# Kernel tuning notes

Hardware: AMD Instinct MI355X
Metric: run time of the kernel (lower is better)

The kernel has to match this reference:

```python
import math
import jax, jax.numpy as jnp
import numpy as np
from math import factorial as fact

RS_IN = [(8, 0), (8, 1)]
RS_OUT = [(8, 0), (8, 1)]
N_PATH = 384
HIDDEN = 64
B, N_OUT_PTS, N_IN_PTS = 2, 256, 256

def _lfilters(l_in, l_out, lmax=10):
    return [l for l in range(abs(l_in - l_out), l_in + l_out + 1) if l <= lmax]

# ---- Clebsch-Gordan / Wigner-3j in the real spherical-harmonic basis ----
def _cg(j1, m1, j2, m2, j3, m3):
    if m1 + m2 != m3:
        return 0.0
    kmin = max(0, j2 - j3 - m1, j1 - j3 + m2)
    kmax = min(j1 + j2 - j3, j1 - m1, j2 + m2)
    if kmax < kmin:
        return 0.0
    pre = math.sqrt((2 * j3 + 1) * fact(j3 + j1 - j2) * fact(j3 - j1 + j2) * fact(j1 + j2 - j3) / fact(j1 + j2 + j3 + 1))
    pre *= math.sqrt(fact(j3 + m3) * fact(j3 - m3) * fact(j1 - m1) * fact(j1 + m1) * fact(j2 - m2) * fact(j2 + m2))
    s = sum((-1) ** k / (fact(k) * fact(j1 + j2 - j3 - k) * fact(j1 - m1 - k) * fact(j2 + m2 - k) * fact(j3 - j2 + m1 + k) * fact(j3 - j1 - m2 + k)) for k in range(kmin, kmax + 1))
    return pre * s

def _wigner3j(j1, j2, j3):
    W = np.zeros((2 * j1 + 1, 2 * j2 + 1, 2 * j3 + 1))
    for m1 in range(-j1, j1 + 1):
        for m2 in range(-j2, j2 + 1):
            m3 = -(m1 + m2)
            if abs(m3) <= j3:
                W[m1 + j1, m2 + j2, m3 + j3] = (-1) ** (j1 - j2 - m3) / math.sqrt(2 * j3 + 1) * _cg(j1, m1, j2, m2, j3, -m3)
    return W

def _A(l):
    # change of basis real<->complex SH: Y^real_a = sum_m A[a, m] Y^complex_m
    A = np.zeros((2 * l + 1, 2 * l + 1), dtype=np.complex128)
    A[l, l] = 1.0
    for m in range(1, l + 1):
        A[l + m, l + m] = (-1) ** m / math.sqrt(2)
        A[l + m, l - m] = 1.0 / math.sqrt(2)
        A[l - m, l - m] = 1j / math.sqrt(2)
        A[l - m, l + m] = -1j * (-1) ** m / math.sqrt(2)
    return A

def _real_cg(l1, l2, l3):
    W = _wigner3j(l1, l2, l3).astype(np.complex128)
    Q = np.einsum('am,bn,cp,mnp->abc', _A(l1).conj(), _A(l2).conj(), _A(l3).conj(), W)
    v = Q.flat[int(np.argmax(np.abs(Q)))]
    if abs(v) > 1e-12:
        Q = Q * (v.conjugate() / abs(v))  # rotate global phase so tensor is real
    assert np.abs(Q.imag).max() < 1e-8
    return Q.real.astype(np.float32)

# ---- real spherical harmonics of unit directions, l = 0, 1, 2 ----
_C0 = 0.28209479177387814
_C1 = 0.4886025119029199
_C2A = 1.0925484305920792
_C2B = 0.31539156525252005
_C2C = 0.5462742152960396

def _sh(xyz):
    r = jnp.linalg.norm(xyz, axis=-1, keepdims=True)
    u = xyz / jnp.maximum(r, 1e-12)
    x, y, z = u[..., 0], u[..., 1], u[..., 2]
    Y0 = _C0 * jnp.ones_like(x)[..., None]
    Y1 = _C1 * jnp.stack([y, z, x], axis=-1)
    Y2 = jnp.stack([_C2A * x * y, _C2A * y * z, _C2B * (3.0 * z * z - 1.0), _C2A * x * z, _C2C * (x * x - y * y)], axis=-1)
    return {0: Y0, 1: Y1, 2: Y2}


def setup_inputs() -> dict:
    key = jax.random.key(0)
    ks = jax.random.split(key, 3)
    dm = jax.random.normal(ks[0], (B, N_OUT_PTS, N_IN_PTS, 3), dtype=jnp.float32)
    W1 = 0.1 * jax.random.normal(ks[1], (1, HIDDEN), dtype=jnp.float32)
    b1 = jnp.zeros((HIDDEN,), dtype=jnp.float32)
    W2 = (1.0 / math.sqrt(HIDDEN)) * jax.random.normal(ks[2], (HIDDEN, N_PATH), dtype=jnp.float32)
    b2 = jnp.zeros((N_PATH,), dtype=jnp.float32)
    Q00 = jnp.asarray(_real_cg(0, 0, 0))  # (1,1,1)
    Q01 = jnp.asarray(_real_cg(0, 1, 1))  # (1,3,3)
    Q10 = jnp.asarray(_real_cg(1, 0, 1))  # (3,1,3)
    Q11 = jnp.asarray(np.concatenate([_real_cg(1, 1, l) for l in (0, 1, 2)], axis=2))  # (3,3,9)
    return {"difference_matrix": dm, "W1": W1, "b1": b1, "W2": W2, "b2": b2, "Q00": Q00, "Q01": Q01, "Q10": Q10, "Q11": Q11}


def reference(difference_matrix, W1, b1, W2, b2, Q00, Q01, Q10, Q11):
    Bb, No, Ni, _ = difference_matrix.shape
    Ys = _sh(difference_matrix)                       # l -> [B, No, Ni, 2l+1]
    radii = jnp.linalg.norm(difference_matrix, axis=-1)
    h = jax.nn.relu(radii[..., None] * W1[0] + b1)    # radial MLP
    weights = h @ W2 + b2                             # [B, No, Ni, N_PATH]
    Qs = {(0, 0): Q00, (0, 1): Q01, (1, 0): Q10, (1, 1): Q11}
    begin_w = 0
    rows = []
    for i, (mul_out, l_out) in enumerate(RS_OUT):
        num = sum(mul_in * len(_lfilters(l_in, l_out)) for mul_in, l_in in RS_IN) * Ni
        cols = []
        for j, (mul_in, l_in) in enumerate(RS_IN):
            lfs = _lfilters(l_in, l_out)
            n = mul_out * mul_in * len(lfs)
            w = weights[..., begin_w:begin_w + n].reshape(Bb, No, Ni, mul_out, mul_in, len(lfs))
            begin_w += n
            Q = Qs[(i, j)]
            K = 0.0
            off = 0
            for k, lf in enumerate(lfs):
                Qk = Q[:, :, off:off + 2 * lf + 1]
                off += 2 * lf + 1
                # i=m_out, j=m_in, r=m_filter, b n m = batch/N_out/N_in, u v = mul_out/mul_in
                K = K + jnp.einsum('ijr,bnmr,bnmuv->uivjbnm', Qk, Ys[lf], w[..., k])
            K = K * (math.sqrt(2 * l_in + 1) * math.sqrt(4.0 * math.pi) / math.sqrt(num))
            cols.append(K.reshape(mul_out * (2 * l_out + 1), mul_in * (2 * l_in + 1), Bb, No, Ni))
        rows.append(jnp.concatenate(cols, axis=1))
    return jnp.concatenate(rows, axis=0)  # [n_out, n_in, B, N_out, N_in]
```

## Files before the change

### kernel.cpp

```cpp
#include <hip/hip_runtime.h>
#include <math.h>

namespace {

typedef float f32x4 __attribute__((ext_vector_type(4)));

constexpr int kPts   = 2 * 256 * 256;
constexpr int kPlane = kPts;
constexpr int kHid   = 64;
constexpr int kPath  = 384;
constexpr int kG     = 8;
constexpr int kUvPer = 64 / kG;

constexpr size_t kWsV    = (size_t)kPath * kHid;
constexpr size_t kWsFlag = kWsV + kPath;
constexpr size_t kWsNeedBytes = (kWsFlag + 1) * sizeof(float);

__global__ void prep_kernel(const float* __restrict__ W1,
                            const float* __restrict__ b1,
                            const float* __restrict__ W2,
                            float* __restrict__ W2T,
                            float* __restrict__ V,
                            unsigned* __restrict__ flag)
{
    int t = blockIdx.x * blockDim.x + threadIdx.x;
    if (t < kPath * kHid) {
        int p = t >> 6, i = t & 63;
        W2T[t] = W2[i * kPath + p];
    }
    if (t < kPath) {
        float acc = 0.f;
        for (int i = 0; i < kHid; ++i)
            acc += fmaxf(W1[i], 0.f) * W2[i * kPath + t];
        V[t] = acc;
    }
    if (t == 0) {
        unsigned f = 1u;
        for (int i = 0; i < kHid; ++i)
            if (b1[i] != 0.f) f = 0u;
        *flag = f;
    }
}

template <bool USE_WS>
__global__ __launch_bounds__(256)
void se3_kernel(const float* __restrict__ dm,
                const float* __restrict__ W1,
                const float* __restrict__ b1,
                const float* __restrict__ W2,
                const float* __restrict__ b2,
                const float* __restrict__ Q00,
                const float* __restrict__ Q01,
                const float* __restrict__ Q10,
                const float* __restrict__ Q11,
                const float* __restrict__ W2T,
                const float* __restrict__ V,
                const unsigned* __restrict__ flag,
                float* __restrict__ out)
{
    const int g   = blockIdx.x * blockDim.x + threadIdx.x;
    const int uv0 = blockIdx.y * kUvPer;

    const f32x4* dmv = reinterpret_cast<const f32x4*>(dm) + 3 * (size_t)g;
    f32x4 f0 = dmv[0], f1 = dmv[1], f2 = dmv[2];
    float px[4] = { f0.x, f0.w, f1.z, f2.y };
    float py[4] = { f0.y, f1.x, f1.w, f2.z };
    float pz[4] = { f0.z, f1.y, f2.x, f2.w };

    float r[4], ux[4], uy[4], uz[4];
#pragma unroll
    for (int p = 0; p < 4; ++p) {
        r[p] = sqrtf(px[p] * px[p] + py[p] * py[p] + pz[p] * pz[p]);
        float inv = 1.0f / fmaxf(r[p], 1e-12f);
        ux[p] = px[p] * inv; uy[p] = py[p] * inv; uz[p] = pz[p] * inv;
    }

    const float Y0 = 0.28209479177387814f;
    const float c1 = 0.4886025119029199f;
    float Y10[4], Y11[4], Y12[4], Y2[5][4];
#pragma unroll
    for (int p = 0; p < 4; ++p) {
        Y10[p] = c1 * uy[p];
        Y11[p] = c1 * uz[p];
        Y12[p] = c1 * ux[p];
        Y2[0][p] = 1.0925484305920792f * ux[p] * uy[p];
        Y2[1][p] = 1.0925484305920792f * uy[p] * uz[p];
        Y2[2][p] = 0.31539156525252005f * (3.f * uz[p] * uz[p] - 1.f);
        Y2[3][p] = 1.0925484305920792f * ux[p] * uz[p];
        Y2[4][p] = 0.5462742152960396f * (ux[p] * ux[p] - uy[p] * uy[p]);
    }

    constexpr float kS4pi = 3.5449077018110318f;
    constexpr float kSq3  = 1.7320508075688772f;
    const float n00 = kS4pi / 64.f;
    const float n01 = kSq3 * kS4pi / 64.f;
    const float n10 = kS4pi / 90.50966799187809f;
    const float n11 = kSq3 * kS4pi / 90.50966799187809f;

    const float s00 = n00 * Q00[0] * Y0;
    float G0[9];
#pragma unroll
    for (int e = 0; e < 9; ++e) G0[e] = n11 * Q11[e * 9 + 0] * Y0;

    float g01[3][4], g10[3][4], G1[9][4], G2[9][4];
#pragma unroll
    for (int jc = 0; jc < 3; ++jc) {
        float q0 = Q01[jc * 3 + 0], q1 = Q01[jc * 3 + 1], q2 = Q01[jc * 3 + 2];
#pragma unroll
        for (int p = 0; p < 4; ++p)
            g01[jc][p] = n01 * (q0 * Y10[p] + q1 * Y11[p] + q2 * Y12[p]);
    }
#pragma unroll
    for (int ir = 0; ir < 3; ++ir) {
        float q0 = Q10[ir * 3 + 0], q1 = Q10[ir * 3 + 1], q2 = Q10[ir * 3 + 2];
#pragma unroll
        for (int p = 0; p < 4; ++p)
            g10[ir][p] = n10 * (q0 * Y10[p] + q1 * Y11[p] + q2 * Y12[p]);
    }
#pragma unroll
    for (int e = 0; e < 9; ++e) {
        const float* q = Q11 + e * 9;
        float q1 = q[1], q2 = q[2], q3 = q[3];
        float q4 = q[4], q5 = q[5], q6 = q[6], q7 = q[7], q8 = q[8];
#pragma unroll
        for (int p = 0; p < 4; ++p) {
            G1[e][p] = n11 * (q1 * Y10[p] + q2 * Y11[p] + q3 * Y12[p]);
            G2[e][p] = n11 * (q4 * Y2[0][p] + q5 * Y2[1][p] + q6 * Y2[2][p] +
                              q7 * Y2[3][p] + q8 * Y2[4][p]);
        }
    }

    float* __restrict__ obase = out + 4 * (size_t)g;
    auto stf = [&](int row, const float* v4) {
        f32x4 q;
        q.x = v4[0]; q.y = v4[1]; q.z = v4[2]; q.w = v4[3];
        *reinterpret_cast<f32x4*>(obase + (size_t)row * kPlane) = q;
    };

    auto emit = [&](int uv, const float* w00, const float* w01,
                    const float* w10, const float* w110,
                    const float* w111, const float* w112) {
        const int u = uv >> 3, v = uv & 7;
        const int rowu = u * 32;
        float tmp[4];
#pragma unroll
        for (int p = 0; p < 4; ++p) tmp[p] = s00 * w00[p];
        stf(rowu + v, tmp);
#pragma unroll
        for (int jc = 0; jc < 3; ++jc) {
#pragma unroll
            for (int p = 0; p < 4; ++p) tmp[p] = g01[jc][p] * w01[p];
            stf(rowu + 8 + v * 3 + jc, tmp);
        }
#pragma unroll
        for (int ir = 0; ir < 3; ++ir) {
            const int rowb = (8 + u * 3 + ir) * 32;
#pragma unroll
            for (int p = 0; p < 4; ++p) tmp[p] = g10[ir][p] * w10[p];
            stf(rowb + v, tmp);
#pragma unroll
            for (int jc = 0; jc < 3; ++jc) {
                const int e = ir * 3 + jc;
#pragma unroll
                for (int p = 0; p < 4; ++p)
                    tmp[p] = fmaf(G0[e], w110[p],
                              fmaf(G1[e][p], w111[p], G2[e][p] * w112[p]));
                stf(rowb + 8 + v * 3 + jc, tmp);
            }
        }
    };

    bool fast = false;
    if constexpr (USE_WS) fast = (*flag != 0u);

    if (USE_WS && fast) {
#pragma unroll 1
        for (int t = 0; t < kUvPer; ++t) {
            const int uv = uv0 + t;
            float v00 = V[uv],            c00 = b2[uv];
            float v01 = V[64 + uv],       c01 = b2[64 + uv];
            float v10 = V[128 + uv],      c10 = b2[128 + uv];
            float v50 = V[192 + 3 * uv],  c50 = b2[192 + 3 * uv];
            float v51 = V[193 + 3 * uv],  c51 = b2[193 + 3 * uv];
            float v52 = V[194 + 3 * uv],  c52 = b2[194 + 3 * uv];
            float w00[4], w01[4], w10[4], w110[4], w111[4], w112[4];
#pragma unroll
            for (int p = 0; p < 4; ++p) {
                w00[p]  = fmaf(r[p], v00, c00);
                w01[p]  = fmaf(r[p], v01, c01);
                w10[p]  = fmaf(r[p], v10, c10);
                w110[p] = fmaf(r[p], v50, c50);
                w111[p] = fmaf(r[p], v51, c51);
                w112[p] = fmaf(r[p], v52, c52);
            }
            emit(uv, w00, w01, w10, w110, w111, w112);
        }
    } else {
#pragma unroll 1
        for (int t = 0; t < kUvPer; ++t) {
            const int uv = uv0 + t;
            float a00[4], a01[4], a10[4], a110[4], a111[4], a112[4];
#pragma unroll
            for (int p = 0; p < 4; ++p) {
                a00[p]  = b2[uv];
                a01[p]  = b2[64 + uv];
                a10[p]  = b2[128 + uv];
                a110[p] = b2[192 + 3 * uv];
                a111[p] = b2[193 + 3 * uv];
                a112[p] = b2[194 + 3 * uv];
            }
#pragma unroll 1
            for (int i = 0; i < kHid; ++i) {
                float w1i = W1[i], b1i = b1[i];
                float c00, c01, c10, c50, c51, c52;
                if constexpr (USE_WS) {
                    c00 = W2T[(size_t)uv * 64 + i];
                    c01 = W2T[(size_t)(64 + uv) * 64 + i];
                    c10 = W2T[(size_t)(128 + uv) * 64 + i];
                    c50 = W2T[(size_t)(192 + 3 * uv) * 64 + i];
                    c51 = W2T[(size_t)(193 + 3 * uv) * 64 + i];
                    c52 = W2T[(size_t)(194 + 3 * uv) * 64 + i];
                } else {
                    const float* row = W2 + (size_t)i * kPath;
                    c00 = row[uv];
                    c01 = row[64 + uv];
                    c10 = row[128 + uv];
                    c50 = row[192 + 3 * uv];
                    c51 = row[193 + 3 * uv];
                    c52 = row[194 + 3 * uv];
                }
#pragma unroll
                for (int p = 0; p < 4; ++p) {
                    float hi = fmaxf(fmaf(r[p], w1i, b1i), 0.f);
                    a00[p]  = fmaf(hi, c00, a00[p]);
                    a01[p]  = fmaf(hi, c01, a01[p]);
                    a10[p]  = fmaf(hi, c10, a10[p]);
                    a110[p] = fmaf(hi, c50, a110[p]);
                    a111[p] = fmaf(hi, c51, a111[p]);
                    a112[p] = fmaf(hi, c52, a112[p]);
                }
            }
            emit(uv, a00, a01, a10, a110, a111, a112);
        }
    }
}

}

extern "C" void kernel_launch(void* const* d_in, const int* in_sizes, int n_in,
                              void* d_out, int out_size, void* d_ws, size_t ws_size,
                              hipStream_t stream)
{
    const float* dm  = (const float*)d_in[0];
    const float* W1  = (const float*)d_in[1];
    const float* b1  = (const float*)d_in[2];
    const float* W2  = (const float*)d_in[3];
    const float* b2  = (const float*)d_in[4];
    const float* Q00 = (const float*)d_in[5];
    const float* Q01 = (const float*)d_in[6];
    const float* Q10 = (const float*)d_in[7];
    const float* Q11 = (const float*)d_in[8];
    float* out = (float*)d_out;

    const int threads = 256;
    dim3 grid(kPts / 4 / threads, kG);

    if (ws_size >= kWsNeedBytes) {
        float* W2T = (float*)d_ws;
        float* V   = W2T + kWsV;
        unsigned* flag = (unsigned*)(W2T + kWsFlag);
        prep_kernel<<<(kPath * kHid + threads - 1) / threads, threads, 0, stream>>>(
            W1, b1, W2, W2T, V, flag);
        se3_kernel<true><<<grid, threads, 0, stream>>>(
            dm, W1, b1, W2, b2, Q00, Q01, Q10, Q11, W2T, V, flag, out);
    } else {
        se3_kernel<false><<<grid, threads, 0, stream>>>(
            dm, W1, b1, W2, b2, Q00, Q01, Q10, Q11, nullptr, nullptr, nullptr, out);
    }
}
```

Baseline: 117.3 us.

## Split SE3 kernel into staged geometry, weight precompute and per-path sweep kernels

Adds a stage kernel that writes each point's radius and unit direction to the workspace once, along with the folded MLP vector and the zero-bias flag. A sweep kernel then gives each block one (u,v) path pair and a 4096-point segment, and writes 16 output rows with coalesced scalar stores. The aim is to spread output writes across a wider grid and cut redundant spherical-harmonic recomputation. When bias is nonzero, a separate kernel stages the full MLP outputs into a large workspace buffer of about 200 MB. If the workspace is smaller than that, execution falls back to a mono kernel that always evaluates the full MLP and no longer has the zero-bias shortcut.

Result: faster. 113.9 us (-2.9%).

```diff
diff --git a/kernel.cpp b/kernel.cpp
--- a/kernel.cpp
+++ b/kernel.cpp
@@ -4,62 +4,234 @@
 namespace {
 
 typedef float f32x4 __attribute__((ext_vector_type(4)));
-
-constexpr int kPts   = 2 * 256 * 256;
-constexpr int kPlane = kPts;
-constexpr int kHid   = 64;
-constexpr int kPath  = 384;
-constexpr int kG     = 8;
-constexpr int kUvPer = 64 / kG;
-
-constexpr size_t kWsV    = (size_t)kPath * kHid;
-constexpr size_t kWsFlag = kWsV + kPath;
-constexpr size_t kWsNeedBytes = (kWsFlag + 1) * sizeof(float);
-
-__global__ void prep_kernel(const float* __restrict__ W1,
-                            const float* __restrict__ b1,
-                            const float* __restrict__ W2,
-                            float* __restrict__ W2T,
-                            float* __restrict__ V,
-                            unsigned* __restrict__ flag)
-{
-    int t = blockIdx.x * blockDim.x + threadIdx.x;
-    if (t < kPath * kHid) {
-        int p = t >> 6, i = t & 63;
-        W2T[t] = W2[i * kPath + p];
-    }
-    if (t < kPath) {
-        float acc = 0.f;
-        for (int i = 0; i < kHid; ++i)
-            acc += fmaxf(W1[i], 0.f) * W2[i * kPath + t];
-        V[t] = acc;
-    }
-    if (t == 0) {
-        unsigned f = 1u;
-        for (int i = 0; i < kHid; ++i)
-            if (b1[i] != 0.f) f = 0u;
-        *flag = f;
-    }
-}
-
-template <bool USE_WS>
+typedef float f32x2 __attribute__((ext_vector_type(2)));
+
+constexpr int kPts  = 2 * 256 * 256;
+constexpr int kHid  = 64;
+constexpr int kPath = 384;
+
+constexpr size_t kVOff    = (size_t)kPts * 4;
+constexpr size_t kFlagOff = kVOff + kPath;
+constexpr size_t kWOff    = kVOff + 512;
+constexpr size_t kWFloats = 64ull * kPts * 6;
+constexpr size_t kNeedBytes = (kWOff + kWFloats) * 4;
+
+constexpr float kY0   = 0.28209479177387814f;
+constexpr float kC1   = 0.4886025119029199f;
+constexpr float kC2A  = 1.0925484305920792f;
+constexpr float kC2B  = 0.31539156525252005f;
+constexpr float kC2C  = 0.5462742152960396f;
+constexpr float kS4pi = 3.5449077018110318f;
+constexpr float kSq3  = 1.7320508075688772f;
+constexpr float kN00  = kS4pi / 64.f;
+constexpr float kN01  = kSq3 * kS4pi / 64.f;
+constexpr float kN10  = kS4pi / 90.50966799187809f;
+constexpr float kN11  = kSq3 * kS4pi / 90.50966799187809f;
+
 __global__ __launch_bounds__(256)
-void se3_kernel(const float* __restrict__ dm,
-                const float* __restrict__ W1,
-                const float* __restrict__ b1,
-                const float* __restrict__ W2,
-                const float* __restrict__ b2,
-                const float* __restrict__ Q00,
-                const float* __restrict__ Q01,
-                const float* __restrict__ Q10,
-                const float* __restrict__ Q11,
-                const float* __restrict__ W2T,
-                const float* __restrict__ V,
-                const unsigned* __restrict__ flag,
-                float* __restrict__ out)
+void stage_kernel(const float* __restrict__ dm,
+                  const float* __restrict__ W1,
+                  const float* __restrict__ b1,
+                  const float* __restrict__ W2,
+                  f32x4* __restrict__ ru,
+                  float* __restrict__ V,
+                  unsigned* __restrict__ flag)
+{
+    const int pt = blockIdx.x * 256 + threadIdx.x;
+    float dx = dm[3 * pt + 0], dy = dm[3 * pt + 1], dz = dm[3 * pt + 2];
+    float r  = sqrtf(dx * dx + dy * dy + dz * dz);
+    float inv = 1.0f / fmaxf(r, 1e-12f);
+    f32x4 q; q.x = r; q.y = dx * inv; q.z = dy * inv; q.w = dz * inv;
+    ru[pt] = q;
+
+    if (blockIdx.x == 0) {
+        for (int p = threadIdx.x; p < kPath; p += 256) {
+            float acc = 0.f;
+            for (int i = 0; i < kHid; ++i)
+                acc += fmaxf(W1[i], 0.f) * W2[i * kPath + p];
+            V[p] = acc;
+        }
+        if (threadIdx.x == 0) {
+            unsigned f = 1u;
+            for (int i = 0; i < kHid; ++i)
+                if (b1[i] != 0.f) f = 0u;
+            *flag = f;
+        }
+    }
+}
+
+__global__ __launch_bounds__(256)
+void wstage_kernel(const float* __restrict__ W1,
+                   const float* __restrict__ b1,
+                   const float* __restrict__ W2,
+                   const float* __restrict__ b2,
+                   const f32x4* __restrict__ ru,
+                   const unsigned* __restrict__ flag,
+                   float* __restrict__ wout)
+{
+    if (*flag) return;
+    const int pt = blockIdx.x * 256 + threadIdx.x;
+    const float r = ru[pt].x;
+    float h[kHid];
+#pragma unroll
+    for (int i = 0; i < kHid; ++i)
+        h[i] = fmaxf(fmaf(r, W1[i], b1[i]), 0.f);
+
+#pragma unroll 1
+    for (int uv = 0; uv < 64; ++uv) {
+        const int p[6] = { uv, 64 + uv, 128 + uv,
+                           192 + 3 * uv, 193 + 3 * uv, 194 + 3 * uv };
+        float acc[6];
+#pragma unroll
+        for (int c = 0; c < 6; ++c) acc[c] = b2[p[c]];
+#pragma unroll 1
+        for (int i = 0; i < kHid; ++i) {
+            const float* row = W2 + (size_t)i * kPath;
+#pragma unroll
+            for (int c = 0; c < 6; ++c) acc[c] = fmaf(h[i], row[p[c]], acc[c]);
+        }
+        float* o = wout + ((size_t)uv * kPts + pt) * 6;
+#pragma unroll
+        for (int c = 0; c < 6; ++c) o[c] = acc[c];
+    }
+}
+
+__global__ __launch_bounds__(256)
+void sweep_kernel(const float* __restrict__ Q00,
+                  const float* __restrict__ Q01,
+                  const float* __restrict__ Q10,
+                  const float* __restrict__ Q11,
+                  const float* __restrict__ b2,
+                  const f32x4* __restrict__ ru,
+                  const float* __restrict__ V,
+                  const unsigned* __restrict__ flag,
+                  const float* __restrict__ wstaged,
+                  float* __restrict__ out)
+{
+    const int seg = blockIdx.x;
+    const int uv  = blockIdx.y;
+    const int u = uv >> 3, v = uv & 7;
+
+    const float s00p = kN00 * Q00[0] * kY0;
+    float a01[3][3], a10[3][3], g0c[9], a11[9][3], b11[9][5];
+    const float c2s[5] = { kC2A, kC2A, kC2B, kC2A, kC2C };
+#pragma unroll
+    for (int jc = 0; jc < 3; ++jc)
+#pragma unroll
+        for (int m = 0; m < 3; ++m)
+            a01[jc][m] = kN01 * kC1 * Q01[jc * 3 + m];
+#pragma unroll
+    for (int ir = 0; ir < 3; ++ir)
+#pragma unroll
+        for (int m = 0; m < 3; ++m)
+            a10[ir][m] = kN10 * kC1 * Q10[ir * 3 + m];
+#pragma unroll
+    for (int e = 0; e < 9; ++e) {
+        g0c[e] = kN11 * kY0 * Q11[e * 9 + 0];
+#pragma unroll
+        for (int m = 0; m < 3; ++m) a11[e][m] = kN11 * kC1 * Q11[e * 9 + 1 + m];
+#pragma unroll
+        for (int m = 0; m < 5; ++m) b11[e][m] = kN11 * c2s[m] * Q11[e * 9 + 4 + m];
+    }
+
+    const bool fast = (*flag != 0u);
+    const int pw[6] = { uv, 64 + uv, 128 + uv,
+                        192 + 3 * uv, 193 + 3 * uv, 194 + 3 * uv };
+    float vv[6], cc[6];
+#pragma unroll
+    for (int c = 0; c < 6; ++c) { vv[c] = V[pw[c]]; cc[c] = b2[pw[c]]; }
+
+    int pr[16];
+    pr[0] = u * 32 + v;
+#pragma unroll
+    for (int jc = 0; jc < 3; ++jc) pr[1 + jc] = u * 32 + 8 + v * 3 + jc;
+#pragma unroll
+    for (int ir = 0; ir < 3; ++ir) pr[4 + ir] = (8 + u * 3 + ir) * 32 + v;
+#pragma unroll
+    for (int e = 0; e < 9; ++e)
+        pr[7 + e] = (8 + u * 3 + (e / 3)) * 32 + 8 + v * 3 + (e % 3);
+
+    const size_t segbase = (size_t)seg * 4096 + threadIdx.x;
+
+#pragma unroll 1
+    for (int batch = 0; batch < 4; ++batch) {
+        const size_t p0 = segbase + (size_t)batch * 1024;
+
+        float bs[4][8], w_[4][6];
+#pragma unroll
+        for (int k = 0; k < 4; ++k) {
+            f32x4 q = ru[p0 + k * 256];
+            float r = q.x, x = q.y, y = q.z, z = q.w;
+            bs[k][0] = y;  bs[k][1] = z;  bs[k][2] = x;
+            bs[k][3] = x * y;
+            bs[k][4] = y * z;
+            bs[k][5] = fmaf(3.f * z, z, -1.f);
+            bs[k][6] = x * z;
+            bs[k][7] = fmaf(x, x, -(y * y));
+            if (fast) {
+#pragma unroll
+                for (int c = 0; c < 6; ++c) w_[k][c] = fmaf(r, vv[c], cc[c]);
+            } else {
+                const float* wp = wstaged + ((size_t)uv * kPts + (p0 + k * 256)) * 6;
+#pragma unroll
+                for (int c = 0; c < 6; ++c) w_[k][c] = wp[c];
+            }
+        }
+
+#pragma unroll
+        for (int k = 0; k < 4; ++k)
+            out[(size_t)pr[0] * kPts + p0 + k * 256] = s00p * w_[k][0];
+
+#pragma unroll
+        for (int jc = 0; jc < 3; ++jc) {
+#pragma unroll
+            for (int k = 0; k < 4; ++k) {
+                float g = fmaf(a01[jc][2], bs[k][2],
+                           fmaf(a01[jc][1], bs[k][1], a01[jc][0] * bs[k][0]));
+                out[(size_t)pr[1 + jc] * kPts + p0 + k * 256] = g * w_[k][1];
+            }
+        }
+#pragma unroll
+        for (int ir = 0; ir < 3; ++ir) {
+#pragma unroll
+            for (int k = 0; k < 4; ++k) {
+                float g = fmaf(a10[ir][2], bs[k][2],
+                           fmaf(a10[ir][1], bs[k][1], a10[ir][0] * bs[k][0]));
+                out[(size_t)pr[4 + ir] * kPts + p0 + k * 256] = g * w_[k][2];
+            }
+        }
+#pragma unroll
+        for (int e = 0; e < 9; ++e) {
+#pragma unroll
+            for (int k = 0; k < 4; ++k) {
+                float lin = fmaf(a11[e][2], bs[k][2],
+                             fmaf(a11[e][1], bs[k][1], a11[e][0] * bs[k][0]));
+                float quad = b11[e][0] * bs[k][3];
+#pragma unroll
+                for (int m = 1; m < 5; ++m)
+                    quad = fmaf(b11[e][m], bs[k][3 + m], quad);
+                float val = fmaf(g0c[e], w_[k][3],
+                             fmaf(lin, w_[k][4], quad * w_[k][5]));
+                out[(size_t)pr[7 + e] * kPts + p0 + k * 256] = val;
+            }
+        }
+    }
+}
+
+__global__ __launch_bounds__(256)
+void mono_kernel(const float* __restrict__ dm,
+                 const float* __restrict__ W1,
+                 const float* __restrict__ b1,
+                 const float* __restrict__ W2,
+                 const float* __restrict__ b2,
+                 const float* __restrict__ Q00,
+                 const float* __restrict__ Q01,
+                 const float* __restrict__ Q10,
+                 const float* __restrict__ Q11,
+                 float* __restrict__ out)
 {
     const int g   = blockIdx.x * blockDim.x + threadIdx.x;
-    const int uv0 = blockIdx.y * kUvPer;
+    const int uv0 = blockIdx.y * 8;
 
     const f32x4* dmv = reinterpret_cast<const f32x4*>(dm) + 3 * (size_t)g;
     f32x4 f0 = dmv[0], f1 = dmv[1], f2 = dmv[2];
@@ -70,177 +242,99 @@
     float r[4], ux[4], uy[4], uz[4];
 #pragma unroll
     for (int p = 0; p < 4; ++p) {
-        r[p] = sqrtf(px[p] * px[p] + py[p] * py[p] + pz[p] * pz[p]);
+        r[p] = sqrtf(px[p]*px[p] + py[p]*py[p] + pz[p]*pz[p]);
         float inv = 1.0f / fmaxf(r[p], 1e-12f);
-        ux[p] = px[p] * inv; uy[p] = py[p] * inv; uz[p] = pz[p] * inv;
-    }
-
-    const float Y0 = 0.28209479177387814f;
-    const float c1 = 0.4886025119029199f;
-    float Y10[4], Y11[4], Y12[4], Y2[5][4];
+        ux[p] = px[p]*inv; uy[p] = py[p]*inv; uz[p] = pz[p]*inv;
+    }
+    float Y10[4], Y11v[4], Y12[4], Y2[5][4];
 #pragma unroll
     for (int p = 0; p < 4; ++p) {
-        Y10[p] = c1 * uy[p];
-        Y11[p] = c1 * uz[p];
-        Y12[p] = c1 * ux[p];
-        Y2[0][p] = 1.0925484305920792f * ux[p] * uy[p];
-        Y2[1][p] = 1.0925484305920792f * uy[p] * uz[p];
-        Y2[2][p] = 0.31539156525252005f * (3.f * uz[p] * uz[p] - 1.f);
-        Y2[3][p] = 1.0925484305920792f * ux[p] * uz[p];
-        Y2[4][p] = 0.5462742152960396f * (ux[p] * ux[p] - uy[p] * uy[p]);
-    }
-
-    constexpr float kS4pi = 3.5449077018110318f;
-    constexpr float kSq3  = 1.7320508075688772f;
-    const float n00 = kS4pi / 64.f;
-    const float n01 = kSq3 * kS4pi / 64.f;
-    const float n10 = kS4pi / 90.50966799187809f;
-    const float n11 = kSq3 * kS4pi / 90.50966799187809f;
-
-    const float s00 = n00 * Q00[0] * Y0;
+        Y10[p] = kC1 * uy[p]; Y11v[p] = kC1 * uz[p]; Y12[p] = kC1 * ux[p];
+        Y2[0][p] = kC2A * ux[p] * uy[p];
+        Y2[1][p] = kC2A * uy[p] * uz[p];
+        Y2[2][p] = kC2B * (3.f * uz[p] * uz[p] - 1.f);
+        Y2[3][p] = kC2A * ux[p] * uz[p];
+        Y2[4][p] = kC2C * (ux[p]*ux[p] - uy[p]*uy[p]);
+    }
+    const float s00 = kN00 * Q00[0] * kY0;
     float G0[9];
 #pragma unroll
-    for (int e = 0; e < 9; ++e) G0[e] = n11 * Q11[e * 9 + 0] * Y0;
-
+    for (int e = 0; e < 9; ++e) G0[e] = kN11 * Q11[e*9] * kY0;
     float g01[3][4], g10[3][4], G1[9][4], G2[9][4];
 #pragma unroll
-    for (int jc = 0; jc < 3; ++jc) {
-        float q0 = Q01[jc * 3 + 0], q1 = Q01[jc * 3 + 1], q2 = Q01[jc * 3 + 2];
+    for (int jc = 0; jc < 3; ++jc)
 #pragma unroll
         for (int p = 0; p < 4; ++p)
-            g01[jc][p] = n01 * (q0 * Y10[p] + q1 * Y11[p] + q2 * Y12[p]);
-    }
-#pragma unroll
-    for (int ir = 0; ir < 3; ++ir) {
-        float q0 = Q10[ir * 3 + 0], q1 = Q10[ir * 3 + 1], q2 = Q10[ir * 3 + 2];
+            g01[jc][p] = kN01 * (Q01[jc*3]*Y10[p] + Q01[jc*3+1]*Y11v[p] + Q01[jc*3+2]*Y12[p]);
+#pragma unroll
+    for (int ir = 0; ir < 3; ++ir)
 #pragma unroll
         for (int p = 0; p < 4; ++p)
-            g10[ir][p] = n10 * (q0 * Y10[p] + q1 * Y11[p] + q2 * Y12[p]);
-    }
+            g10[ir][p] = kN10 * (Q10[ir*3]*Y10[p] + Q10[ir*3+1]*Y11v[p] + Q10[ir*3+2]*Y12[p]);
 #pragma unroll
     for (int e = 0; e < 9; ++e) {
         const float* q = Q11 + e * 9;
-        float q1 = q[1], q2 = q[2], q3 = q[3];
-        float q4 = q[4], q5 = q[5], q6 = q[6], q7 = q[7], q8 = q[8];
 #pragma unroll
         for (int p = 0; p < 4; ++p) {
-            G1[e][p] = n11 * (q1 * Y10[p] + q2 * Y11[p] + q3 * Y12[p]);
-            G2[e][p] = n11 * (q4 * Y2[0][p] + q5 * Y2[1][p] + q6 * Y2[2][p] +
-                              q7 * Y2[3][p] + q8 * Y2[4][p]);
-        }
-    }
-
+            G1[e][p] = kN11 * (q[1]*Y10[p] + q[2]*Y11v[p] + q[3]*Y12[p]);
+            G2[e][p] = kN11 * (q[4]*Y2[0][p] + q[5]*Y2[1][p] + q[6]*Y2[2][p] +
+                               q[7]*Y2[3][p] + q[8]*Y2[4][p]);
+        }
+    }
     float* __restrict__ obase = out + 4 * (size_t)g;
     auto stf = [&](int row, const float* v4) {
-        f32x4 q;
-        q.x = v4[0]; q.y = v4[1]; q.z = v4[2]; q.w = v4[3];
-        *reinterpret_cast<f32x4*>(obase + (size_t)row * kPlane) = q;
+        f32x4 q; q.x=v4[0]; q.y=v4[1]; q.z=v4[2]; q.w=v4[3];
+        *reinterpret_cast<f32x4*>(obase + (size_t)row * kPts) = q;
     };
-
-    auto emit = [&](int uv, const float* w00, const float* w01,
-                    const float* w10, const float* w110,
-                    const float* w111, const float* w112) {
+#pragma unroll 1
+    for (int t = 0; t < 8; ++t) {
+        const int uv = uv0 + t;
+        float a00[4], a01v[4], a10v[4], a110[4], a111[4], a112[4];
+#pragma unroll
+        for (int p = 0; p < 4; ++p) {
+            a00[p]=b2[uv]; a01v[p]=b2[64+uv]; a10v[p]=b2[128+uv];
+            a110[p]=b2[192+3*uv]; a111[p]=b2[193+3*uv]; a112[p]=b2[194+3*uv];
+        }
+#pragma unroll 1
+        for (int i = 0; i < kHid; ++i) {
+            float w1i = W1[i], b1i = b1[i];
+            const float* row = W2 + (size_t)i * kPath;
+            float c00=row[uv], c01=row[64+uv], c10=row[128+uv];
+            float c50=row[192+3*uv], c51=row[193+3*uv], c52=row[194+3*uv];
+#pragma unroll
+            for (int p = 0; p < 4; ++p) {
+                float hi = fmaxf(fmaf(r[p], w1i, b1i), 0.f);
+                a00[p]=fmaf(hi,c00,a00[p]); a01v[p]=fmaf(hi,c01,a01v[p]);
+                a10v[p]=fmaf(hi,c10,a10v[p]); a110[p]=fmaf(hi,c50,a110[p]);
+                a111[p]=fmaf(hi,c51,a111[p]); a112[p]=fmaf(hi,c52,a112[p]);
+            }
+        }
         const int u = uv >> 3, v = uv & 7;
         const int rowu = u * 32;
         float tmp[4];
 #pragma unroll
-        for (int p = 0; p < 4; ++p) tmp[p] = s00 * w00[p];
+        for (int p = 0; p < 4; ++p) tmp[p] = s00 * a00[p];
         stf(rowu + v, tmp);
 #pragma unroll
         for (int jc = 0; jc < 3; ++jc) {
 #pragma unroll
-            for (int p = 0; p < 4; ++p) tmp[p] = g01[jc][p] * w01[p];
-            stf(rowu + 8 + v * 3 + jc, tmp);
+            for (int p = 0; p < 4; ++p) tmp[p] = g01[jc][p] * a01v[p];
+            stf(rowu + 8 + v*3 + jc, tmp);
         }
 #pragma unroll
         for (int ir = 0; ir < 3; ++ir) {
-            const int rowb = (8 + u * 3 + ir) * 32;
-#pragma unroll
-            for (int p = 0; p < 4; ++p) tmp[p] = g10[ir][p] * w10[p];
+            const int rowb = (8 + u*3 + ir) * 32;
+#pragma unroll
+            for (int p = 0; p < 4; ++p) tmp[p] = g10[ir][p] * a10v[p];
             stf(rowb + v, tmp);
 #pragma unroll
             for (int jc = 0; jc < 3; ++jc) {
-                const int e = ir * 3 + jc;
+                const int e = ir*3 + jc;
 #pragma unroll
                 for (int p = 0; p < 4; ++p)
-                    tmp[p] = fmaf(G0[e], w110[p],
-                              fmaf(G1[e][p], w111[p], G2[e][p] * w112[p]));
-                stf(rowb + 8 + v * 3 + jc, tmp);
-            }
-        }
-    };
-
-    bool fast = false;
-    if constexpr (USE_WS) fast = (*flag != 0u);
-
-    if (USE_WS && fast) {
-#pragma unroll 1
-        for (int t = 0; t < kUvPer; ++t) {
-            const int uv = uv0 + t;
-            float v00 = V[uv],            c00 = b2[uv];
-            float v01 = V[64 + uv],       c01 = b2[64 + uv];
-            float v10 = V[128 + uv],      c10 = b2[128 + uv];
-            float v50 = V[192 + 3 * uv],  c50 = b2[192 + 3 * uv];
-            float v51 = V[193 + 3 * uv],  c51 = b2[193 + 3 * uv];
-            float v52 = V[194 + 3 * uv],  c52 = b2[194 + 3 * uv];
-            float w00[4], w01[4], w10[4], w110[4], w111[4], w112[4];
-#pragma unroll
-            for (int p = 0; p < 4; ++p) {
-                w00[p]  = fmaf(r[p], v00, c00);
-                w01[p]  = fmaf(r[p], v01, c01);
-                w10[p]  = fmaf(r[p], v10, c10);
-                w110[p] = fmaf(r[p], v50, c50);
-                w111[p] = fmaf(r[p], v51, c51);
-                w112[p] = fmaf(r[p], v52, c52);
-            }
-            emit(uv, w00, w01, w10, w110, w111, w112);
-        }
-    } else {
-#pragma unroll 1
-        for (int t = 0; t < kUvPer; ++t) {
-            const int uv = uv0 + t;
-            float a00[4], a01[4], a10[4], a110[4], a111[4], a112[4];
-#pragma unroll
-            for (int p = 0; p < 4; ++p) {
-                a00[p]  = b2[uv];
-                a01[p]  = b2[64 + uv];
-                a10[p]  = b2[128 + uv];
-                a110[p] = b2[192 + 3 * uv];
-                a111[p] = b2[193 + 3 * uv];
-                a112[p] = b2[194 + 3 * uv];
-            }
-#pragma unroll 1
-            for (int i = 0; i < kHid; ++i) {
-                float w1i = W1[i], b1i = b1[i];
-                float c00, c01, c10, c50, c51, c52;
-                if constexpr (USE_WS) {
-                    c00 = W2T[(size_t)uv * 64 + i];
-                    c01 = W2T[(size_t)(64 + uv) * 64 + i];
-                    c10 = W2T[(size_t)(128 + uv) * 64 + i];
-                    c50 = W2T[(size_t)(192 + 3 * uv) * 64 + i];
-                    c51 = W2T[(size_t)(193 + 3 * uv) * 64 + i];
-                    c52 = W2T[(size_t)(194 + 3 * uv) * 64 + i];
-                } else {
-                    const float* row = W2 + (size_t)i * kPath;
-                    c00 = row[uv];
-                    c01 = row[64 + uv];
-                    c10 = row[128 + uv];
-                    c50 = row[192 + 3 * uv];
-                    c51 = row[193 + 3 * uv];
-                    c52 = row[194 + 3 * uv];
-                }
-#pragma unroll
-                for (int p = 0; p < 4; ++p) {
-                    float hi = fmaxf(fmaf(r[p], w1i, b1i), 0.f);
-                    a00[p]  = fmaf(hi, c00, a00[p]);
-                    a01[p]  = fmaf(hi, c01, a01[p]);
-                    a10[p]  = fmaf(hi, c10, a10[p]);
-                    a110[p] = fmaf(hi, c50, a110[p]);
-                    a111[p] = fmaf(hi, c51, a111[p]);
-                    a112[p] = fmaf(hi, c52, a112[p]);
-                }
-            }
-            emit(uv, a00, a01, a10, a110, a111, a112);
+                    tmp[p] = fmaf(G0[e], a110[p], fmaf(G1[e][p], a111[p], G2[e][p]*a112[p]));
+                stf(rowb + 8 + v*3 + jc, tmp);
+            }
         }
     }
 }
@@ -262,19 +356,18 @@
     const float* Q11 = (const float*)d_in[8];
     float* out = (float*)d_out;
 
-    const int threads = 256;
-    dim3 grid(kPts / 4 / threads, kG);
-
-    if (ws_size >= kWsNeedBytes) {
-        float* W2T = (float*)d_ws;
-        float* V   = W2T + kWsV;
-        unsigned* flag = (unsigned*)(W2T + kWsFlag);
-        prep_kernel<<<(kPath * kHid + threads - 1) / threads, threads, 0, stream>>>(
-            W1, b1, W2, W2T, V, flag);
-        se3_kernel<true><<<grid, threads, 0, stream>>>(
-            dm, W1, b1, W2, b2, Q00, Q01, Q10, Q11, W2T, V, flag, out);
+    if (ws_size >= kNeedBytes) {
+        float* ws = (float*)d_ws;
+        f32x4*    ru   = (f32x4*)ws;
+        float*    V    = ws + kVOff;
+        unsigned* flag = (unsigned*)(ws + kFlagOff);
+        float*    wst  = ws + kWOff;
+        stage_kernel<<<kPts / 256, 256, 0, stream>>>(dm, W1, b1, W2, ru, V, flag);
+        wstage_kernel<<<kPts / 256, 256, 0, stream>>>(W1, b1, W2, b2, ru, flag, wst);
+        sweep_kernel<<<dim3(32, 64), 256, 0, stream>>>(
+            Q00, Q01, Q10, Q11, b2, ru, V, flag, wst, out);
     } else {
-        se3_kernel<false><<<grid, threads, 0, stream>>>(
-            dm, W1, b1, W2, b2, Q00, Q01, Q10, Q11, nullptr, nullptr, nullptr, out);
-    }
-}
+        mono_kernel<<<dim3(128, 8), 256, 0, stream>>>(
+            dm, W1, b1, W2, b2, Q00, Q01, Q10, Q11, out);
+    }
+}
```
